# Optimization experiments

Measured on AMD Instinct MI355X. Metric: run time of the kernel, lower is better.

The kernel has to match this reference:

```python
import jax, jax.numpy as jnp
import numpy as np

K_HEADS = 8
D_HEAD = 8
C_IN = 128   # c_x + c_t after channel concat
C_OUT = K_HEADS * D_HEAD  # 64
SMALL = -32767.0  # -2**15 + 1


def setup_inputs() -> dict:
    key = jax.random.key(0)
    ks = jax.random.split(key, 12)
    B, Cx, V, T = 8, 64, 200, 128
    x = jax.random.normal(ks[0], (B, Cx, V, T), dtype=jnp.float32)
    tem_embedding = jax.random.normal(ks[1], (B, Cx, V, T), dtype=jnp.float32)
    s = 0.05
    Wq = jax.random.normal(ks[2], (C_OUT, C_IN), dtype=jnp.float32) * s
    bq = jax.random.normal(ks[3], (C_OUT,), dtype=jnp.float32) * s
    Wk = jax.random.normal(ks[4], (C_OUT, C_IN), dtype=jnp.float32) * s
    bk = jax.random.normal(ks[5], (C_OUT,), dtype=jnp.float32) * s
    Wv = jax.random.normal(ks[6], (C_OUT, C_IN), dtype=jnp.float32) * s
    bv = jax.random.normal(ks[7], (C_OUT,), dtype=jnp.float32) * s
    Wo = jax.random.normal(ks[8], (C_OUT, C_OUT), dtype=jnp.float32) * s
    bo = jax.random.normal(ks[9], (C_OUT,), dtype=jnp.float32) * s
    return {"x": x, "tem_embedding": tem_embedding,
            "Wq": Wq, "bq": bq, "Wk": Wk, "bk": bk,
            "Wv": Wv, "bv": bv, "Wo": Wo, "bo": bo}


def reference(x, tem_embedding, Wq, bq, Wk, bk, Wv, bv, Wo, bo):
    B, _, V, T = x.shape
    # concat temporal embedding on channel dim (last T steps)
    xt = jnp.concatenate([x, tem_embedding[:, :, :, -T:]], axis=1)  # [B, C_IN, V, T]

    def proj(W, b):  # 1x1 conv == channel einsum
        return jnp.einsum('oi,bivt->bovt', W, xt) + b[None, :, None, None]

    def heads(t):  # [B, K*d, V, T] -> [K*B, V, T, d] (split on dim1, cat on dim0)
        t = t.reshape(B, K_HEADS, D_HEAD, V, T)
        t = jnp.transpose(t, (1, 0, 3, 4, 2))  # [K, B, V, T, d]
        return t.reshape(K_HEADS * B, V, T, D_HEAD)

    q = heads(proj(Wq, bq))
    k = heads(proj(Wk, bk))
    v = heads(proj(Wv, bv))

    attn = jnp.einsum('nvtd,nvsd->nvts', q, k) / jnp.sqrt(jnp.float32(D_HEAD))
    causal = jnp.tril(jnp.ones((T, T), dtype=bool))  # [T, T]
    attn = jnp.where(causal[None, None, :, :], attn, SMALL)
    attn = jax.nn.softmax(attn, axis=-1)
    out = jnp.einsum('nvts,nvsd->nvtd', attn, v)  # [K*B, V, T, d]

    # merge heads back: [K*B, V, T, d] -> [B, K*d, V, T]
    out = out.reshape(K_HEADS, B, V, T, D_HEAD)
    out = jnp.transpose(out, (1, 0, 4, 2, 3)).reshape(B, K_HEADS * D_HEAD, V, T)
    out = jnp.einsum('oi,bivt->bovt', Wo, out) + bo[None, :, None, None]
    return jax.nn.relu(out)
```

## Files before the change

### kernel.cpp

```cpp
#include <hip/hip_runtime.h>
#include <stdint.h>

#define TPB 512

constexpr int Bb   = 8;
constexpr int Vv   = 200;
constexpr int Tt   = 128;
constexpr int CIN  = 128;
constexpr int COUT = 64;

typedef __attribute__((ext_vector_type(8))) short bf16x8;
typedef __attribute__((ext_vector_type(4))) short short4v;
typedef __attribute__((ext_vector_type(4))) float f32x4;

__device__ __forceinline__ unsigned short f2bf(float f) {
    union { float f; unsigned u; } x; x.f = f;
    unsigned r = x.u + 0x7fffu + ((x.u >> 16) & 1u);
    return (unsigned short)(r >> 16);
}
__device__ __forceinline__ unsigned pk2(float a, float b) {
    return (unsigned)f2bf(a) | ((unsigned)f2bf(b) << 16);
}

#if __has_builtin(__builtin_amdgcn_mfma_f32_16x16x16bf16_1k)
#define MFMA16(a, b, c) __builtin_amdgcn_mfma_f32_16x16x16bf16_1k(a, b, c, 0, 0, 0)
#else
__device__ __forceinline__ f32x4 mfma16_asm(short4v a, short4v b, f32x4 c) {
    f32x4 d;
    asm("v_mfma_f32_16x16x16_bf16 %0, %1, %2, %3" : "=v"(d) : "v"(a), "v"(b), "v"(c));
    return d;
}
#define MFMA16(a, b, c) mfma16_asm(a, b, c)
#endif

__global__ void prep_w(const float* __restrict__ Wq, const float* __restrict__ Wk,
                       const float* __restrict__ Wv, const float* __restrict__ Wo,
                       unsigned short* __restrict__ ws) {
    int i = blockIdx.x * 256 + threadIdx.x;
    float v;
    if (i < 8192)       v = Wq[i];
    else if (i < 16384) v = Wk[i - 8192];
    else if (i < 24576) v = Wv[i - 16384];
    else                v = Wo[i - 24576];
    ws[i] = f2bf(v);
}

__global__ __launch_bounds__(TPB, 4)
void tatt_fused(const float* __restrict__ x, const float* __restrict__ tem,
                const float* __restrict__ bq, const float* __restrict__ bk,
                const float* __restrict__ bv, const float* __restrict__ bo,
                const unsigned short* __restrict__ ws,
                float* __restrict__ out)
{
    __shared__ __align__(16) unsigned char smem[65536];
    unsigned short* qk = (unsigned short*)smem;
    unsigned short* vt = (unsigned short*)(smem + 32768);
    unsigned short* xt = (unsigned short*)(smem + 49152);
    unsigned short* ot = (unsigned short*)(smem + 49152);

    const int tid = threadIdx.x;
    const int w = tid >> 6, lane = tid & 63;
    const int l15 = lane & 15, qd = lane >> 4;
    const int b = blockIdx.x / Vv, v = blockIdx.x % Vv;
    const float QS = 1.44269504088896f * 0.35355339059327f;

    const float* bpa[3] = {bq, bk, bv};

    for (int half = 0; half < 2; ++half) {
        __syncthreads();
        #pragma unroll
        for (int k = 0; k < 4; ++k) {
            int idx = tid + k * TPB;
            int c = idx & 127, t4 = idx >> 7;
            const float* src = (c < 64 ? x : tem)
                + ((b * 64 + (c & 63)) * Vv + v) * Tt + half * 64 + t4 * 4;
            float4 f = *(const float4*)src;
            float fv[4] = {f.x, f.y, f.z, f.w};
            #pragma unroll
            for (int j = 0; j < 4; ++j) {
                int t = t4 * 4 + j;
                xt[t * CIN + (((c >> 3) ^ (t & 15)) << 3) + (c & 7)] = f2bf(fv[j]);
            }
        }
        __syncthreads();
        #pragma unroll
        for (int j = 0; j < 6; ++j) {
            int tile = w * 6 + j;
            int p = tile >> 4, rem = tile & 15;
            int ot_ = rem & 3, tt = rem >> 2;
            f32x4 acc = {0.f, 0.f, 0.f, 0.f};
            const unsigned short* Wb  = ws + p * 8192 + (ot_ * 16 + l15) * CIN + qd * 8;
            const unsigned short* Bbp = xt + (tt * 16 + l15) * CIN;
            #pragma unroll
            for (int kc = 0; kc < 4; ++kc) {
                bf16x8 a = *(const bf16x8*)(Wb + kc * 32);
                int phys = (kc * 4 + qd) ^ l15;
                bf16x8 bbv = *(const bf16x8*)(Bbp + phys * 8);
                acc = __builtin_amdgcn_mfma_f32_16x16x32_bf16(a, bbv, acc, 0, 0, 0);
            }
            int obase = ot_ * 16 + qd * 4;
            float4 bias = *(const float4*)(bpa[p] + obase);
            float bb4[4] = {bias.x, bias.y, bias.z, bias.w};
            int tg = half * 64 + tt * 16 + l15;
            if (p == 2) {
                #pragma unroll
                for (int r = 0; r < 4; ++r) {
                    int dg = obase + r;
                    int tp = tg ^ ((((dg >> 2) & 3)) << 4);
                    vt[dg * 128 + tp] = f2bf(acc[r] + bb4[r]);
                }
            } else {
                float sc = (p == 0) ? QS : 1.0f;
                ushort4 st4;
                st4.x = f2bf((acc[0] + bb4[0]) * sc);
                st4.y = f2bf((acc[1] + bb4[1]) * sc);
                st4.z = f2bf((acc[2] + bb4[2]) * sc);
                st4.w = f2bf((acc[3] + bb4[3]) * sc);
                int phys = (obase >> 2) ^ (tg & 14);
                *(ushort4*)(qk + p * 8192 + tg * 64 + phys * 4) = st4;
            }
        }
    }
    __syncthreads();

    {
        const int h = w;
        short4v vfrag[8];
        {
            int dg = h * 8 + l15;
            int swz = ((dg >> 2) & 3) << 4;
            #pragma unroll
            for (int st = 0; st < 8; ++st) {
                short4v f = {0, 0, 0, 0};
                if (l15 < 8) {
                    int sp = (st * 16 + qd * 4) ^ swz;
                    f = *(const short4v*)(vt + dg * 128 + sp);
                }
                vfrag[st] = f;
            }
        }
        bool dmask[4];
        #pragma unroll
        for (int r = 0; r < 4; ++r) dmask[r] = (qd * 4 + r) <= l15;
        const int qkoff = ((h * 2) ^ (l15 & 14)) << 2;

        for (int tt = 0; tt < 8; ++tt) {
            bf16x8 qf = {0, 0, 0, 0, 0, 0, 0, 0};
            if (qd == 0) qf = *(const bf16x8*)(qk + (tt * 16 + l15) * 64 + qkoff);
            f32x4 o0 = {0.f, 0.f, 0.f, 0.f}, o1 = {0.f, 0.f, 0.f, 0.f};
            float lac = 0.f;
            #pragma unroll
            for (int st = 0; st < 8; ++st) {
                if (st <= tt) {
                    bf16x8 kf = {0, 0, 0, 0, 0, 0, 0, 0};
                    if (qd == 0) kf = *(const bf16x8*)(qk + 8192 + (st * 16 + l15) * 64 + qkoff);
                    f32x4 z = {0.f, 0.f, 0.f, 0.f};
                    f32x4 s = __builtin_amdgcn_mfma_f32_16x16x32_bf16(kf, qf, z, 0, 0, 0);
                    float p0 = __builtin_amdgcn_exp2f(s[0]);
                    float p1 = __builtin_amdgcn_exp2f(s[1]);
                    float p2 = __builtin_amdgcn_exp2f(s[2]);
                    float p3 = __builtin_amdgcn_exp2f(s[3]);
                    if (st == tt) {
                        p0 = dmask[0] ? p0 : 0.f;
                        p1 = dmask[1] ? p1 : 0.f;
                        p2 = dmask[2] ? p2 : 0.f;
                        p3 = dmask[3] ? p3 : 0.f;
                    }
                    lac += (p0 + p1) + (p2 + p3);
                    int pp0 = (int)pk2(p0, p1), pp1 = (int)pk2(p2, p3);
                    short4v pf;
                    pf[0] = (short)(pp0 & 0xffff); pf[1] = (short)(pp0 >> 16);
                    pf[2] = (short)(pp1 & 0xffff); pf[3] = (short)(pp1 >> 16);
                    if (st & 1) o1 = MFMA16(vfrag[st], pf, o1);
                    else        o0 = MFMA16(vfrag[st], pf, o0);
                }
            }
            float l = lac;
            l += __shfl_xor(l, 16, 64);
            l += __shfl_xor(l, 32, 64);
            float rl = __builtin_amdgcn_rcpf(l);
            if (qd < 2) {
                float r0 = (o0[0] + o1[0]) * rl, r1 = (o0[1] + o1[1]) * rl;
                float r2 = (o0[2] + o1[2]) * rl, r3 = (o0[3] + o1[3]) * rl;
                int t = tt * 16 + l15;
                uint2 st2;
                st2.x = pk2(r0, r1);
                st2.y = pk2(r2, r3);
                *(uint2*)(ot + t * 64 + (((h * 2 + qd) ^ (l15 & 14)) << 2)) = st2;
            }
        }
    }
    __syncthreads();

    {
        const int tt = w;
        #pragma unroll
        for (int ot_ = 0; ot_ < 4; ++ot_) {
            f32x4 acc = {0.f, 0.f, 0.f, 0.f};
            const unsigned short* Ab = ws + 24576 + (ot_ * 16 + l15) * COUT + qd * 8;
            #pragma unroll
            for (int kc = 0; kc < 2; ++kc) {
                bf16x8 a = *(const bf16x8*)(Ab + kc * 32);
                bf16x8 bbv = *(const bf16x8*)(ot + (tt * 16 + l15) * 64
                                 + (((kc * 8 + qd * 2) ^ (l15 & 14)) << 2));
                acc = __builtin_amdgcn_mfma_f32_16x16x32_bf16(a, bbv, acc, 0, 0, 0);
            }
            int obase = ot_ * 16 + qd * 4;
            float4 bias = *(const float4*)(bo + obase);
            float bb4[4] = {bias.x, bias.y, bias.z, bias.w};
            int t = tt * 16 + l15;
            #pragma unroll
            for (int r = 0; r < 4; ++r) {
                float val = acc[r] + bb4[r];
                out[((b * COUT + obase + r) * Vv + v) * Tt + t] = val > 0.f ? val : 0.f;
            }
        }
    }
}

extern "C" void kernel_launch(void* const* d_in, const int* in_sizes, int n_in,
                              void* d_out, int out_size, void* d_ws, size_t ws_size,
                              hipStream_t stream) {
    (void)in_sizes; (void)n_in; (void)ws_size; (void)out_size;
    const float* x   = (const float*)d_in[0];
    const float* tem = (const float*)d_in[1];
    const float* Wq  = (const float*)d_in[2];
    const float* bq  = (const float*)d_in[3];
    const float* Wk  = (const float*)d_in[4];
    const float* bk  = (const float*)d_in[5];
    const float* Wv  = (const float*)d_in[6];
    const float* bv  = (const float*)d_in[7];
    const float* Wo  = (const float*)d_in[8];
    const float* bo  = (const float*)d_in[9];
    float* out = (float*)d_out;
    unsigned short* ws = (unsigned short*)d_ws;

    prep_w<<<dim3(112), dim3(256), 0, stream>>>(Wq, Wk, Wv, Wo, ws);
    tatt_fused<<<dim3(Bb * Vv), dim3(TPB), 0, stream>>>(
        x, tem, bq, bk, bv, bo, ws, out);
}
```

Before: 269.6 us.

## Stream projection in 16-step chunks, shrink LDS, use K=16 MFMA for scores

The projection phase now loads and converts the input 16 time steps at a time, prefetching the next chunk into registers while the current one is multiplied. Each wave handles one or two 16-wide output tiles per chunk, alternating assignments to balance work. This shrinks the staging buffer, and the output tile now reuses the V region after an added barrier. Shared memory drops from 64KB to 52KB and launch bounds rise to 6 blocks per CU, aiming at higher occupancy. QK scores switch from a half-zero 16x16x32 MFMA to a 16x16x16 MFMA that loads only 4-element fragments. The cost is many more barriers (eight chunk rounds instead of two halves) and tighter register limits.

```diff
diff --git a/kernel.cpp b/kernel.cpp
--- a/kernel.cpp
+++ b/kernel.cpp
@@ -45,18 +45,18 @@
     ws[i] = f2bf(v);
 }
 
-__global__ __launch_bounds__(TPB, 4)
+__global__ __launch_bounds__(TPB, 6)
 void tatt_fused(const float* __restrict__ x, const float* __restrict__ tem,
                 const float* __restrict__ bq, const float* __restrict__ bk,
                 const float* __restrict__ bv, const float* __restrict__ bo,
                 const unsigned short* __restrict__ ws,
                 float* __restrict__ out)
 {
-    __shared__ __align__(16) unsigned char smem[65536];
+    __shared__ __align__(16) unsigned char smem[53248];
     unsigned short* qk = (unsigned short*)smem;
     unsigned short* vt = (unsigned short*)(smem + 32768);
+    unsigned short* ot = (unsigned short*)(smem + 32768);
     unsigned short* xt = (unsigned short*)(smem + 49152);
-    unsigned short* ot = (unsigned short*)(smem + 49152);
 
     const int tid = threadIdx.x;
     const int w = tid >> 6, lane = tid & 63;
@@ -64,33 +64,20 @@
     const int b = blockIdx.x / Vv, v = blockIdx.x % Vv;
     const float QS = 1.44269504088896f * 0.35355339059327f;
 
-    const float* bpa[3] = {bq, bk, bv};
-
-    for (int half = 0; half < 2; ++half) {
-        __syncthreads();
-        #pragma unroll
-        for (int k = 0; k < 4; ++k) {
-            int idx = tid + k * TPB;
-            int c = idx & 127, t4 = idx >> 7;
-            const float* src = (c < 64 ? x : tem)
-                + ((b * 64 + (c & 63)) * Vv + v) * Tt + half * 64 + t4 * 4;
-            float4 f = *(const float4*)src;
-            float fv[4] = {f.x, f.y, f.z, f.w};
-            #pragma unroll
-            for (int j = 0; j < 4; ++j) {
-                int t = t4 * 4 + j;
-                xt[t * CIN + (((c >> 3) ^ (t & 15)) << 3) + (c & 7)] = f2bf(fv[j]);
-            }
-        }
-        __syncthreads();
-        #pragma unroll
-        for (int j = 0; j < 6; ++j) {
-            int tile = w * 6 + j;
-            int p = tile >> 4, rem = tile & 15;
-            int ot_ = rem & 3, tt = rem >> 2;
+    {
+        const int tl = tid & 15, cq = tid >> 4;
+        const int c0 = cq * 4;
+        const float* sbase = (c0 < 64 ? x : tem)
+            + ((b * 64 + (c0 & 63)) * Vv + v) * Tt + tl;
+        constexpr int CS = Vv * Tt;
+        float c0v = sbase[0], c1v = sbase[CS], c2v = sbase[2 * CS], c3v = sbase[3 * CS];
+        const int xoff = tl * CIN + ((((c0 >> 3) ^ tl) << 3) + (c0 & 7));
+
+        auto tile_mfma = [&](int tile, int r) {
+            const int p = tile >> 2, ot_ = tile & 3;
             f32x4 acc = {0.f, 0.f, 0.f, 0.f};
             const unsigned short* Wb  = ws + p * 8192 + (ot_ * 16 + l15) * CIN + qd * 8;
-            const unsigned short* Bbp = xt + (tt * 16 + l15) * CIN;
+            const unsigned short* Bbp = xt + l15 * CIN;
             #pragma unroll
             for (int kc = 0; kc < 4; ++kc) {
                 bf16x8 a = *(const bf16x8*)(Wb + kc * 32);
@@ -98,27 +85,44 @@
                 bf16x8 bbv = *(const bf16x8*)(Bbp + phys * 8);
                 acc = __builtin_amdgcn_mfma_f32_16x16x32_bf16(a, bbv, acc, 0, 0, 0);
             }
-            int obase = ot_ * 16 + qd * 4;
-            float4 bias = *(const float4*)(bpa[p] + obase);
+            const int obase = ot_ * 16 + qd * 4;
+            const float* bp = (p == 0) ? bq : (p == 1 ? bk : bv);
+            float4 bias = *(const float4*)(bp + obase);
             float bb4[4] = {bias.x, bias.y, bias.z, bias.w};
-            int tg = half * 64 + tt * 16 + l15;
+            const int tg = r * 16 + l15;
             if (p == 2) {
                 #pragma unroll
-                for (int r = 0; r < 4; ++r) {
-                    int dg = obase + r;
+                for (int rr = 0; rr < 4; ++rr) {
+                    int dg = obase + rr;
                     int tp = tg ^ ((((dg >> 2) & 3)) << 4);
-                    vt[dg * 128 + tp] = f2bf(acc[r] + bb4[r]);
+                    vt[dg * 128 + tp] = f2bf(acc[rr] + bb4[rr]);
                 }
             } else {
                 float sc = (p == 0) ? QS : 1.0f;
-                ushort4 st4;
-                st4.x = f2bf((acc[0] + bb4[0]) * sc);
-                st4.y = f2bf((acc[1] + bb4[1]) * sc);
-                st4.z = f2bf((acc[2] + bb4[2]) * sc);
-                st4.w = f2bf((acc[3] + bb4[3]) * sc);
+                ushort4 s4;
+                s4.x = f2bf((acc[0] + bb4[0]) * sc);
+                s4.y = f2bf((acc[1] + bb4[1]) * sc);
+                s4.z = f2bf((acc[2] + bb4[2]) * sc);
+                s4.w = f2bf((acc[3] + bb4[3]) * sc);
                 int phys = (obase >> 2) ^ (tg & 14);
-                *(ushort4*)(qk + p * 8192 + tg * 64 + phys * 4) = st4;
-            }
+                *(ushort4*)(qk + p * 8192 + tg * 64 + phys * 4) = s4;
+            }
+        };
+
+        for (int r = 0; r < 8; ++r) {
+            if (r) __syncthreads();
+            ushort4 s4;
+            s4.x = f2bf(c0v); s4.y = f2bf(c1v); s4.z = f2bf(c2v); s4.w = f2bf(c3v);
+            *(ushort4*)(xt + xoff) = s4;
+            if (r < 7) {
+                int o = (r + 1) * 16;
+                c0v = sbase[o];          c1v = sbase[CS + o];
+                c2v = sbase[2 * CS + o]; c3v = sbase[3 * CS + o];
+            }
+            __syncthreads();
+            const int wr = (w + ((r & 1) << 2)) & 7;
+            tile_mfma(wr, r);
+            if (wr < 4) tile_mfma(8 + wr, r);
         }
     }
     __syncthreads();
@@ -127,8 +131,8 @@
         const int h = w;
         short4v vfrag[8];
         {
-            int dg = h * 8 + l15;
-            int swz = ((dg >> 2) & 3) << 4;
+            const int dg = h * 8 + l15;
+            const int swz = ((dg >> 2) & 3) << 4;
             #pragma unroll
             for (int st = 0; st < 8; ++st) {
                 short4v f = {0, 0, 0, 0};
@@ -139,23 +143,25 @@
                 vfrag[st] = f;
             }
         }
+        __syncthreads();
+
         bool dmask[4];
         #pragma unroll
         for (int r = 0; r < 4; ++r) dmask[r] = (qd * 4 + r) <= l15;
-        const int qkoff = ((h * 2) ^ (l15 & 14)) << 2;
+        const int qkoff = ((h * 2 + qd) ^ (l15 & 14)) << 2;
 
         for (int tt = 0; tt < 8; ++tt) {
-            bf16x8 qf = {0, 0, 0, 0, 0, 0, 0, 0};
-            if (qd == 0) qf = *(const bf16x8*)(qk + (tt * 16 + l15) * 64 + qkoff);
+            short4v qf = {0, 0, 0, 0};
+            if (qd < 2) qf = *(const short4v*)(qk + (tt * 16 + l15) * 64 + qkoff);
             f32x4 o0 = {0.f, 0.f, 0.f, 0.f}, o1 = {0.f, 0.f, 0.f, 0.f};
             float lac = 0.f;
             #pragma unroll
             for (int st = 0; st < 8; ++st) {
                 if (st <= tt) {
-                    bf16x8 kf = {0, 0, 0, 0, 0, 0, 0, 0};
-                    if (qd == 0) kf = *(const bf16x8*)(qk + 8192 + (st * 16 + l15) * 64 + qkoff);
+                    short4v kf = {0, 0, 0, 0};
+                    if (qd < 2) kf = *(const short4v*)(qk + 8192 + (st * 16 + l15) * 64 + qkoff);
                     f32x4 z = {0.f, 0.f, 0.f, 0.f};
-                    f32x4 s = __builtin_amdgcn_mfma_f32_16x16x32_bf16(kf, qf, z, 0, 0, 0);
+                    f32x4 s = MFMA16(kf, qf, z);
                     float p0 = __builtin_amdgcn_exp2f(s[0]);
                     float p1 = __builtin_amdgcn_exp2f(s[1]);
                     float p2 = __builtin_amdgcn_exp2f(s[2]);
```

Measured after the change: 252.1 us. -6.5%, faster.
